# Performance work log

Measured on AMD Instinct MI355X. Metric: run time of the kernel, lower is better.

## Reference

```python
import jax, jax.numpy as jnp
import numpy as np
import math

NUM_BUCKETS = 32
MAX_DISTANCE = 128
N_HEADS = 16
HEAD_DIM = 64


def _relative_position_bucket(relative_position, num_buckets=NUM_BUCKETS, max_distance=MAX_DISTANCE):
    # bidirectional (encoder): half the buckets for positive positions
    nb = num_buckets // 2
    rel_buckets = (relative_position > 0).astype(jnp.int32) * nb
    rp = jnp.abs(relative_position)
    max_exact = nb // 2
    is_small = rp < max_exact
    rp_large = max_exact + (
        jnp.log(jnp.maximum(rp, 1).astype(jnp.float32) / max_exact)
        / math.log(max_distance / max_exact)
        * (nb - max_exact)
    ).astype(jnp.int32)
    rp_large = jnp.minimum(rp_large, nb - 1)
    return rel_buckets + jnp.where(is_small, rp, rp_large)


def setup_inputs() -> dict:
    key = jax.random.key(0)
    ks = jax.random.split(key, 6)
    d_model = 1024
    B, S = 4, 2048
    scale = 1.0 / math.sqrt(d_model)
    return {
        "hidden_states": jax.random.normal(ks[0], (B, S, d_model), jnp.float32),
        "Wq": jax.random.normal(ks[1], (d_model, N_HEADS * HEAD_DIM), jnp.float32) * scale,
        "Wk": jax.random.normal(ks[2], (d_model, N_HEADS * HEAD_DIM), jnp.float32) * scale,
        "Wv": jax.random.normal(ks[3], (d_model, N_HEADS * HEAD_DIM), jnp.float32) * scale,
        "Wo": jax.random.normal(ks[4], (N_HEADS * HEAD_DIM, d_model), jnp.float32) * scale,
        "rel_bias_table": jax.random.normal(ks[5], (NUM_BUCKETS, N_HEADS), jnp.float32),
    }


def reference(hidden_states, Wq, Wk, Wv, Wo, rel_bias_table):
    B, S, _ = hidden_states.shape
    # projections -> [B, H, S, hd]
    def proj(W):
        return jnp.einsum('bsd,df->bsf', hidden_states, W).reshape(B, S, N_HEADS, HEAD_DIM).transpose(0, 2, 1, 3)
    q = proj(Wq)
    k = proj(Wk)
    v = proj(Wv)

    # relative position bias: [1, H, S, S]
    ctx = jnp.arange(S)[:, None]
    mem = jnp.arange(S)[None, :]
    buckets = _relative_position_bucket(mem - ctx)  # [S, S] int32
    position_bias = rel_bias_table[buckets].transpose(2, 0, 1)[None]  # [1, H, S, S]

    # scaling = 1.0 in MT5Attention (d_kv**-0.5 baked into init elsewhere)
    attn_weights = jnp.einsum('bhqd,bhkd->bhqk', q, k) + position_bias
    attn_weights = jax.nn.softmax(attn_weights, axis=-1)
    attn_output = jnp.einsum('bhqk,bhkd->bqhd', attn_weights, v).reshape(B, S, N_HEADS * HEAD_DIM)
    attn_output = jnp.einsum('bsf,fd->bsd', attn_output, Wo)
    return attn_output, position_bias, attn_weights
```

## Files before the change

kernel.cpp:

```cpp
#include <hip/hip_runtime.h>
#include <cstdint>
#include <cmath>

#define NH 16
#define HD 64
#define SQ 2048
#define NB 4
#define DM 1024

typedef _Float16 half_t;
typedef _Float16 h8 __attribute__((ext_vector_type(8)));
typedef _Float16 h4 __attribute__((ext_vector_type(4)));
typedef float f4 __attribute__((ext_vector_type(4)));

__device__ __forceinline__ int rel_bucket(int delta) {
    int b = (delta > 0) ? 16 : 0;
    int a = (delta < 0) ? -delta : delta;
    if (a < 8) return b + a;
    int large = 8 + (int)(__logf((float)a * 0.125f) * 2.8853900817779268f);
    return b + (large < 15 ? large : 15);
}

__device__ __forceinline__ void gl_lds(const half_t* g, half_t* l) {
    __builtin_amdgcn_global_load_lds((const __attribute__((address_space(1))) unsigned int*)g,
                                     (__attribute__((address_space(3))) unsigned int*)l, 16, 0, 0);
}

__global__ __launch_bounds__(256) void prep(const float* __restrict__ X,
                                            const float* __restrict__ Wq,
                                            const float* __restrict__ Wk,
                                            const float* __restrict__ Wv,
                                            const float* __restrict__ Wo,
                                            const float* __restrict__ table,
                                            half_t* __restrict__ Xh, half_t* __restrict__ Wqt,
                                            half_t* __restrict__ Wkt, half_t* __restrict__ Wvt,
                                            half_t* __restrict__ Wot, float* __restrict__ dtab) {
    const int id = blockIdx.x;
    if (id < 4096) {
        size_t i = ((size_t)id * 256 + threadIdx.x) * 8;
        float4 a = *(const float4*)&X[i];
        float4 b = *(const float4*)&X[i + 4];
        half_t t[8] = {(half_t)a.x, (half_t)a.y, (half_t)a.z, (half_t)a.w,
                       (half_t)b.x, (half_t)b.y, (half_t)b.z, (half_t)b.w};
        *(h8*)&Xh[i] = *(h8*)t;
        return;
    }
    if (id >= 5120) {
        const int h = id - 5120;
        for (int d = threadIdx.x; d < 4095; d += 256)
            dtab[h * 4096 + d] = table[rel_bucket(d - 2047) * NH + h];
        return;
    }
    __shared__ float T[64][65];
    const int t = id - 4096;
    const int which = t >> 8, tile = t & 255;
    const float* W = which == 0 ? Wq : which == 1 ? Wk : which == 2 ? Wv : Wo;
    half_t* Wt = which == 0 ? Wqt : which == 1 ? Wkt : which == 2 ? Wvt : Wot;
    const int k0 = (tile >> 4) * 64, n0 = (tile & 15) * 64;
    const int c = threadIdx.x & 63, rr = threadIdx.x >> 6;
    for (int r = rr; r < 64; r += 4) T[r][c] = W[(size_t)(k0 + r) * DM + n0 + c];
    __syncthreads();
    for (int r = rr; r < 64; r += 4) Wt[(size_t)(n0 + r) * DM + k0 + c] = (half_t)T[c][r];
}

__global__ __launch_bounds__(256) void transpose_v(const half_t* __restrict__ v,
                                                   half_t* __restrict__ vT) {
    __shared__ half_t T[64][72];
    const int bh = blockIdx.y, j0 = blockIdx.x * 64;
    const size_t base = (size_t)bh * (SQ * HD);
    const int t = threadIdx.x;
    for (int e = t; e < 512; e += 256) {
        int r = e >> 3, c = e & 7;
        *(h8*)&T[r][c * 8] = *(const h8*)&v[base + (size_t)(j0 + r) * HD + c * 8];
    }
    __syncthreads();
    const int d = t & 63, jc = t >> 6;
    half_t tmp[16];
#pragma unroll
    for (int jj = 0; jj < 16; ++jj) tmp[jj] = T[jc * 16 + jj][d];
    *(h8*)&vT[base + (size_t)d * SQ + j0 + jc * 16] = *(h8*)&tmp[0];
    *(h8*)&vT[base + (size_t)d * SQ + j0 + jc * 16 + 8] = *(h8*)&tmp[8];
}

__global__ __launch_bounds__(256) void mm_qkv(const half_t* __restrict__ A,
                                              const half_t* __restrict__ Wqt,
                                              const half_t* __restrict__ Wkt,
                                              const half_t* __restrict__ Wvt,
                                              half_t* __restrict__ qo, half_t* __restrict__ ko,
                                              half_t* __restrict__ vo) {
    const int z = blockIdx.z;
    const half_t* Bt = z == 0 ? Wqt : z == 1 ? Wkt : Wvt;
    half_t* outp = z == 0 ? qo : z == 1 ? ko : vo;
    __shared__ half_t Al[2][4096];
    __shared__ half_t Bl[2][4096];
    const int tid = threadIdx.x;
    const int lane = tid & 63, w = tid >> 6;
    const int wr = w >> 1, wc = w & 1;
    const int id0 = blockIdx.y * 8 + blockIdx.x;
    const int swz = (id0 & 7) * 64 + (id0 >> 3);
    const int m0 = (swz >> 3) * 128, n0 = (swz & 7) * 128;

    f4 acc[4][4];
#pragma unroll
    for (int i = 0; i < 4; ++i)
#pragma unroll
        for (int j = 0; j < 4; ++j) acc[i][j] = (f4){0.f, 0.f, 0.f, 0.f};

    const int kc = lane >> 4;
    const int srl = lane >> 2;
    const int sc = lane & 3;

    auto stage = [&](int buf, int k0) {
#pragma unroll
        for (int inst = 0; inst < 2; ++inst) {
            int r = w * 32 + inst * 16 + srl;
            int cg = sc ^ ((r >> 1) & 3);
            gl_lds(&A[(size_t)(m0 + r) * DM + k0 + cg * 8], &Al[buf][(w * 32 + inst * 16) * 32]);
            gl_lds(&Bt[(size_t)(n0 + r) * DM + k0 + cg * 8], &Bl[buf][(w * 32 + inst * 16) * 32]);
        }
    };

    stage(0, 0);
    __syncthreads();
    int cur = 0;
    for (int t = 0; t < 32; ++t) {
        if (t < 31) stage(cur ^ 1, (t + 1) * 32);
        h8 af[4], bf[4];
#pragma unroll
        for (int ms = 0; ms < 4; ++ms) {
            int r = wr * 64 + ms * 16 + (lane & 15);
            af[ms] = *(const h8*)&Al[cur][r * 32 + ((kc ^ ((r >> 1) & 3)) * 8)];
        }
#pragma unroll
        for (int ns = 0; ns < 4; ++ns) {
            int r = wc * 64 + ns * 16 + (lane & 15);
            bf[ns] = *(const h8*)&Bl[cur][r * 32 + ((kc ^ ((r >> 1) & 3)) * 8)];
        }
#pragma unroll
        for (int ms = 0; ms < 4; ++ms)
#pragma unroll
            for (int ns = 0; ns < 4; ++ns)
                acc[ms][ns] =
                    __builtin_amdgcn_mfma_f32_16x16x32_f16(bf[ns], af[ms], acc[ms][ns], 0, 0, 0);
        __syncthreads();
        cur ^= 1;
    }

#pragma unroll
    for (int ms = 0; ms < 4; ++ms)
#pragma unroll
        for (int ns = 0; ns < 4; ++ns) {
            int m = m0 + wr * 64 + ms * 16 + (lane & 15);
            int nb = n0 + wc * 64 + ns * 16 + ((lane >> 4) << 2);
            int b = m >> 11, s = m & 2047, h = nb >> 6, d = nb & 63;
            h4 ph = {(half_t)acc[ms][ns][0], (half_t)acc[ms][ns][1], (half_t)acc[ms][ns][2],
                     (half_t)acc[ms][ns][3]};
            *(h4*)&outp[((size_t)(b * NH + h) * SQ + s) * HD + d] = ph;
        }
}

__global__ __launch_bounds__(256) void mm_wo(const half_t* __restrict__ A,
                                             const half_t* __restrict__ Bt,
                                             float* __restrict__ outp) {
    __shared__ half_t Al[2][4096];
    __shared__ half_t Bl[2][4096];
    const int tid = threadIdx.x;
    const int lane = tid & 63, w = tid >> 6;
    const int wr = w >> 1, wc = w & 1;
    const int id0 = blockIdx.y * 8 + blockIdx.x;
    const int swz = (id0 & 7) * 64 + (id0 >> 3);
    const int m0 = (swz >> 3) * 128, n0 = (swz & 7) * 128;

    f4 acc[4][4];
#pragma unroll
    for (int i = 0; i < 4; ++i)
#pragma unroll
        for (int j = 0; j < 4; ++j) acc[i][j] = (f4){0.f, 0.f, 0.f, 0.f};

    const int kc = lane >> 4;
    const int srl = lane >> 2;
    const int sc = lane & 3;

    auto stage = [&](int buf, int k0) {
#pragma unroll
        for (int inst = 0; inst < 2; ++inst) {
            int r = w * 32 + inst * 16 + srl;
            int cg = sc ^ ((r >> 1) & 3);
            gl_lds(&A[(size_t)(m0 + r) * DM + k0 + cg * 8], &Al[buf][(w * 32 + inst * 16) * 32]);
            gl_lds(&Bt[(size_t)(n0 + r) * DM + k0 + cg * 8], &Bl[buf][(w * 32 + inst * 16) * 32]);
        }
    };

    stage(0, 0);
    __syncthreads();
    int cur = 0;
    for (int t = 0; t < 32; ++t) {
        if (t < 31) stage(cur ^ 1, (t + 1) * 32);
        h8 af[4], bf[4];
#pragma unroll
        for (int ms = 0; ms < 4; ++ms) {
            int r = wr * 64 + ms * 16 + (lane & 15);
            af[ms] = *(const h8*)&Al[cur][r * 32 + ((kc ^ ((r >> 1) & 3)) * 8)];
        }
#pragma unroll
        for (int ns = 0; ns < 4; ++ns) {
            int r = wc * 64 + ns * 16 + (lane & 15);
            bf[ns] = *(const h8*)&Bl[cur][r * 32 + ((kc ^ ((r >> 1) & 3)) * 8)];
        }
#pragma unroll
        for (int ms = 0; ms < 4; ++ms)
#pragma unroll
            for (int ns = 0; ns < 4; ++ns)
                acc[ms][ns] =
                    __builtin_amdgcn_mfma_f32_16x16x32_f16(bf[ns], af[ms], acc[ms][ns], 0, 0, 0);
        __syncthreads();
        cur ^= 1;
    }

#pragma unroll
    for (int ms = 0; ms < 4; ++ms)
#pragma unroll
        for (int ns = 0; ns < 4; ++ns) {
            int m = m0 + wr * 64 + ms * 16 + (lane & 15);
            int nb = n0 + wc * 64 + ns * 16 + ((lane >> 4) << 2);
            __builtin_nontemporal_store(acc[ms][ns], (f4*)&outp[(size_t)m * DM + nb]);
        }
}

__global__ __launch_bounds__(256) void fused_attn(const half_t* __restrict__ q,
                                                  const half_t* __restrict__ k,
                                                  const half_t* __restrict__ vT,
                                                  const float* __restrict__ table,
                                                  float* __restrict__ attw,
                                                  half_t* __restrict__ ctx) {
    __shared__ float biasE[2176];
    __shared__ char Psm[16384];
    __shared__ half_t Kl[2][4096];
    __shared__ half_t Vl[2][4096];
    const int tid = threadIdx.x, lane = tid & 63, w = tid >> 6;

    const int id = blockIdx.x;
    const int idx = (id & 7) * 128 + (id >> 3);
    const int bh = idx >> 4, i0 = (idx & 15) * 128;
    const int h = bh & 15, b = bh >> 4;
    const size_t qb = (size_t)bh * (SQ * HD);
    const half_t* kb = k + qb;
    const half_t* vb = vT + qb;

    for (int t = tid; t < 2176; t += 256)
        biasE[t] = __expf(table[rel_bucket(t - i0 - 127) * NH + h]);

    h8 qf[2][2];
#pragma unroll
    for (int isub = 0; isub < 2; ++isub) {
        const half_t* qp =
            &q[qb + (size_t)(i0 + w * 32 + isub * 16 + (lane & 15)) * HD + (lane >> 4) * 8];
        qf[isub][0] = *(const h8*)qp;
        qf[isub][1] = *(const h8*)(qp + 32);
    }

    const int sr = lane >> 3;
    const int sc = lane & 7;

    auto stageK = [&](int buf, int j0) {
#pragma unroll
        for (int inst = 0; inst < 2; ++inst) {
            int r = w * 16 + inst * 8 + sr;
            gl_lds(&kb[(size_t)(j0 + r) * HD + ((sc ^ (r & 7)) * 8)],
                   &Kl[buf][(w * 16 + inst * 8) * 64]);
        }
    };
    auto stageV = [&](int buf, int j0) {
#pragma unroll
        for (int inst = 0; inst < 2; ++inst) {
            int r = w * 16 + inst * 8 + sr;
            gl_lds(&vb[(size_t)r * SQ + j0 + ((sc ^ (r & 7)) * 8)],
                   &Vl[buf][(w * 16 + inst * 8) * 64]);
        }
    };

    stageK(0, 0);
    __syncthreads();
    float srow[2] = {0.f, 0.f};
    int cur = 0;
    for (int t = 0; t < 32; ++t) {
        const int j0 = t * 64;
        if (t < 31) stageK(cur ^ 1, j0 + 64);
#pragma unroll
        for (int ns = 0; ns < 4; ++ns) {
            const int rr = ns * 16 + (lane & 15);
            const int kc = lane >> 4;
            h8 kf0 = *(const h8*)&Kl[cur][rr * 64 + ((kc ^ (rr & 7)) * 8)];
            h8 kf1 = *(const h8*)&Kl[cur][rr * 64 + (((kc + 4) ^ (rr & 7)) * 8)];
#pragma unroll
            for (int isub = 0; isub < 2; ++isub) {
                f4 z = (f4){0.f, 0.f, 0.f, 0.f};
                z = __builtin_amdgcn_mfma_f32_16x16x32_f16(kf0, qf[isub][0], z, 0, 0, 0);
                z = __builtin_amdgcn_mfma_f32_16x16x32_f16(kf1, qf[isub][1], z, 0, 0, 0);
                int u0 =
                    j0 + ns * 16 + ((lane >> 4) << 2) - (w * 32 + isub * 16 + (lane & 15)) + 127;
#pragma unroll
                for (int reg = 0; reg < 4; ++reg)
                    srow[isub] = fmaf(__expf(z[reg]), biasE[u0 + reg], srow[isub]);
            }
        }
        __syncthreads();
        cur ^= 1;
    }
    float sinv[2];
#pragma unroll
    for (int isub = 0; isub < 2; ++isub) {
        float s = srow[isub];
        s += __shfl_xor(s, 16);
        s += __shfl_xor(s, 32);
        sinv[isub] = 1.0f / s;
    }

    f4 o[4][2];
#pragma unroll
    for (int ns = 0; ns < 4; ++ns)
#pragma unroll
        for (int isub = 0; isub < 2; ++isub) o[ns][isub] = (f4){0.f, 0.f, 0.f, 0.f};
    const size_t awb = (size_t)bh * ((size_t)SQ * SQ);
    char* Pw = Psm + w * 4096;

    stageK(0, 0);
    stageV(0, 0);
    __syncthreads();
    cur = 0;
    for (int t = 0; t < 32; ++t) {
        const int j0 = t * 64;
        if (t < 31) {
            stageK(cur ^ 1, j0 + 64);
            stageV(cur ^ 1, j0 + 64);
        }
        __builtin_amdgcn_sched_barrier(0);
        f4 a[4][2];
#pragma unroll
        for (int ns = 0; ns < 4; ++ns) {
            const int rr = ns * 16 + (lane & 15);
            const int kc = lane >> 4;
            h8 kf0 = *(const h8*)&Kl[cur][rr * 64 + ((kc ^ (rr & 7)) * 8)];
            h8 kf1 = *(const h8*)&Kl[cur][rr * 64 + (((kc + 4) ^ (rr & 7)) * 8)];
#pragma unroll
            for (int isub = 0; isub < 2; ++isub) {
                f4 z = (f4){0.f, 0.f, 0.f, 0.f};
                z = __builtin_amdgcn_mfma_f32_16x16x32_f16(kf0, qf[isub][0], z, 0, 0, 0);
                z = __builtin_amdgcn_mfma_f32_16x16x32_f16(kf1, qf[isub][1], z, 0, 0, 0);
                a[ns][isub] = z;
            }
        }
#pragma unroll
        for (int ns = 0; ns < 4; ++ns)
#pragma unroll
            for (int isub = 0; isub < 2; ++isub) {
                const int wloc = w * 32 + isub * 16 + (lane & 15);
                const int jbase = ns * 16 + ((lane >> 4) << 2);
                const int u0 = j0 + jbase - wloc + 127;
                f4 p;
#pragma unroll
                for (int reg = 0; reg < 4; ++reg)
                    p[reg] = __expf(a[ns][isub][reg]) * biasE[u0 + reg] * sinv[isub];
                __builtin_nontemporal_store(p,
                                            (f4*)&attw[awb + (size_t)(i0 + wloc) * SQ + j0 + jbase]);
                const int iloc = isub * 16 + (lane & 15);
                h4 ph = {(half_t)p[0], (half_t)p[1], (half_t)p[2], (half_t)p[3]};
                *(h4*)&Pw[iloc * 128 + (((jbase >> 3) ^ (iloc & 7)) << 4) + ((jbase & 4) << 1)] = ph;
            }
        h8 pf[2][2];
#pragma unroll
        for (int isub = 0; isub < 2; ++isub) {
            const int iloc = isub * 16 + (lane & 15);
            pf[isub][0] = *(const h8*)&Pw[iloc * 128 + (((lane >> 4) ^ (iloc & 7)) << 4)];
            pf[isub][1] = *(const h8*)&Pw[iloc * 128 + ((((lane >> 4) + 4) ^ (iloc & 7)) << 4)];
        }
#pragma unroll
        for (int ns = 0; ns < 4; ++ns) {
            const int rr = ns * 16 + (lane & 15);
            const int kc = lane >> 4;
            h8 vf0 = *(const h8*)&Vl[cur][rr * 64 + ((kc ^ (rr & 7)) * 8)];
            h8 vf1 = *(const h8*)&Vl[cur][rr * 64 + (((kc + 4) ^ (rr & 7)) * 8)];
#pragma unroll
            for (int isub = 0; isub < 2; ++isub) {
                o[ns][isub] =
                    __builtin_amdgcn_mfma_f32_16x16x32_f16(pf[isub][0], vf0, o[ns][isub], 0, 0, 0);
                o[ns][isub] =
                    __builtin_amdgcn_mfma_f32_16x16x32_f16(pf[isub][1], vf1, o[ns][isub], 0, 0, 0);
            }
        }
        asm volatile("s_waitcnt vmcnt(8)" ::: "memory");
        __builtin_amdgcn_s_barrier();
        __builtin_amdgcn_sched_barrier(0);
        cur ^= 1;
    }
#pragma unroll
    for (int ns = 0; ns < 4; ++ns)
#pragma unroll
        for (int isub = 0; isub < 2; ++isub)
#pragma unroll
            for (int reg = 0; reg < 4; ++reg) {
                int row = i0 + w * 32 + isub * 16 + (lane >> 4) * 4 + reg;
                int d = ns * 16 + (lane & 15);
                ctx[((size_t)(b * SQ + row)) * DM + h * HD + d] = (half_t)o[ns][isub][reg];
            }
}

__global__ __launch_bounds__(256) void bias_fill(const float* __restrict__ dtab,
                                                 float* __restrict__ pb) {
    __shared__ float L[2052];
    const int i = blockIdx.x, h = blockIdx.y;
    const int s0 = 2047 - i, a0 = s0 & ~3, sh = s0 - a0;
    for (int t = threadIdx.x * 4; t < 2052; t += 1024)
        *(f4*)&L[t] = *(const f4*)&dtab[h * 4096 + a0 + t];
    __syncthreads();
    const size_t base = ((size_t)h * SQ + i) * SQ;
#pragma unroll
    for (int half = 0; half < 2; ++half) {
        int j = half * 1024 + threadIdx.x * 4;
        f4 o = {L[sh + j], L[sh + j + 1], L[sh + j + 2], L[sh + j + 3]};
        __builtin_nontemporal_store(o, (f4*)&pb[base + j]);
    }
}

extern "C" void kernel_launch(void* const* d_in, const int* in_sizes, int n_in, void* d_out,
                              int out_size, void* d_ws, size_t ws_size, hipStream_t stream) {
    const float* X = (const float*)d_in[0];
    const float* Wq = (const float*)d_in[1];
    const float* Wk = (const float*)d_in[2];
    const float* Wv = (const float*)d_in[3];
    const float* Wo = (const float*)d_in[4];
    const float* tbl = (const float*)d_in[5];

    float* out = (float*)d_out;
    float* attn_out = out;
    float* pb = out + (size_t)NB * SQ * DM;
    float* attw = pb + (size_t)NH * SQ * SQ;

    const size_t need_bytes = 109314048;
    half_t* hb = (ws_size >= need_bytes) ? (half_t*)d_ws : (half_t*)pb;
    half_t* Xh = hb;
    half_t* qh = hb + 8388608;
    half_t* kh = hb + 16777216;
    half_t* vh = hb + 25165824;
    half_t* vTh = hb + 33554432;
    half_t* ctxh = hb + 41943040;
    half_t* Wqt = hb + 50331648;
    half_t* Wkt = hb + 51380224;
    half_t* Wvt = hb + 52428800;
    half_t* Wot = hb + 53477376;
    float* dtab = (float*)(hb + 54525952);

    dim3 blk(256);
    prep<<<dim3(5136), blk, 0, stream>>>(X, Wq, Wk, Wv, Wo, tbl, Xh, Wqt, Wkt, Wvt, Wot, dtab);
    mm_qkv<<<dim3(8, 64, 3), blk, 0, stream>>>(Xh, Wqt, Wkt, Wvt, qh, kh, vh);
    transpose_v<<<dim3(32, 64), blk, 0, stream>>>(vh, vTh);
    fused_attn<<<dim3(1024), blk, 0, stream>>>(qh, kh, vTh, tbl, attw, ctxh);
    mm_wo<<<dim3(8, 64), blk, 0, stream>>>(ctxh, Wot, attn_out);
    bias_fill<<<dim3(SQ, NH), blk, 0, stream>>>(dtab, pb);
}
```

Measured before the change: 542.6 us.

## Fuse V transpose into QKV GEMM, keep P in registers, merge Wo with bias fill

The QKV GEMM now writes V directly in transposed layout for the z==2 slice, so the separate transpose kernel is gone. The attention kernel keeps P in registers by permuting the K row layout to match the MFMA operand pattern, which removes the LDS P round trip and frees 16KB of shared memory. It also reads precomputed exp-bias entries from dtab and sets launch bounds for 3 blocks per CU. The Wo GEMM and the position-bias fill are merged into one launch so the memory-bound fill can overlap the GEMM; the swizzle changes raise the risk of layout bugs.

```diff
diff --git a/kernel.cpp b/kernel.cpp
--- a/kernel.cpp
+++ b/kernel.cpp
@@ -11,6 +11,7 @@
 typedef _Float16 half_t;
 typedef _Float16 h8 __attribute__((ext_vector_type(8)));
 typedef _Float16 h4 __attribute__((ext_vector_type(4)));
+typedef _Float16 h2 __attribute__((ext_vector_type(2)));
 typedef float f4 __attribute__((ext_vector_type(4)));
 
 __device__ __forceinline__ int rel_bucket(int delta) {
@@ -25,6 +26,16 @@
     __builtin_amdgcn_global_load_lds((const __attribute__((address_space(1))) unsigned int*)g,
                                      (__attribute__((address_space(3))) unsigned int*)l, 16, 0, 0);
 }
+
+__device__ __forceinline__ h2 pkrtz(float a, float b) {
+    auto r = __builtin_amdgcn_cvt_pkrtz(a, b);
+    return *(h2*)&r;
+}
+
+union PFU {
+    h2 x[4];
+    h8 v;
+};
 
 __global__ __launch_bounds__(256) void prep(const float* __restrict__ X,
                                             const float* __restrict__ Wq,
@@ -47,7 +58,7 @@
     }
     if (id >= 5120) {
         const int h = id - 5120;
-        for (int d = threadIdx.x; d < 4095; d += 256)
+        for (int d = threadIdx.x; d < 4096; d += 256)
             dtab[h * 4096 + d] = table[rel_bucket(d - 2047) * NH + h];
         return;
     }
@@ -63,34 +74,14 @@
     for (int r = rr; r < 64; r += 4) Wt[(size_t)(n0 + r) * DM + k0 + c] = (half_t)T[c][r];
 }
 
-__global__ __launch_bounds__(256) void transpose_v(const half_t* __restrict__ v,
-                                                   half_t* __restrict__ vT) {
-    __shared__ half_t T[64][72];
-    const int bh = blockIdx.y, j0 = blockIdx.x * 64;
-    const size_t base = (size_t)bh * (SQ * HD);
-    const int t = threadIdx.x;
-    for (int e = t; e < 512; e += 256) {
-        int r = e >> 3, c = e & 7;
-        *(h8*)&T[r][c * 8] = *(const h8*)&v[base + (size_t)(j0 + r) * HD + c * 8];
-    }
-    __syncthreads();
-    const int d = t & 63, jc = t >> 6;
-    half_t tmp[16];
-#pragma unroll
-    for (int jj = 0; jj < 16; ++jj) tmp[jj] = T[jc * 16 + jj][d];
-    *(h8*)&vT[base + (size_t)d * SQ + j0 + jc * 16] = *(h8*)&tmp[0];
-    *(h8*)&vT[base + (size_t)d * SQ + j0 + jc * 16 + 8] = *(h8*)&tmp[8];
-}
-
 __global__ __launch_bounds__(256) void mm_qkv(const half_t* __restrict__ A,
                                               const half_t* __restrict__ Wqt,
                                               const half_t* __restrict__ Wkt,
                                               const half_t* __restrict__ Wvt,
                                               half_t* __restrict__ qo, half_t* __restrict__ ko,
-                                              half_t* __restrict__ vo) {
+                                              half_t* __restrict__ vTo) {
     const int z = blockIdx.z;
-    const half_t* Bt = z == 0 ? Wqt : z == 1 ? Wkt : Wvt;
-    half_t* outp = z == 0 ? qo : z == 1 ? ko : vo;
+    const half_t* Bt = z == 0 ? Wqt : (z == 1 ? Wkt : Wvt);
     __shared__ half_t Al[2][4096];
     __shared__ half_t Bl[2][4096];
     const int tid = threadIdx.x;
@@ -100,12 +91,6 @@
     const int swz = (id0 & 7) * 64 + (id0 >> 3);
     const int m0 = (swz >> 3) * 128, n0 = (swz & 7) * 128;
 
-    f4 acc[4][4];
-#pragma unroll
-    for (int i = 0; i < 4; ++i)
-#pragma unroll
-        for (int j = 0; j < 4; ++j) acc[i][j] = (f4){0.f, 0.f, 0.f, 0.f};
-
     const int kc = lane >> 4;
     const int srl = lane >> 2;
     const int sc = lane & 3;
@@ -120,121 +105,94 @@
         }
     };
 
+    f4 acc[4][4];
+#pragma unroll
+    for (int i = 0; i < 4; ++i)
+#pragma unroll
+        for (int j = 0; j < 4; ++j) acc[i][j] = (f4){0.f, 0.f, 0.f, 0.f};
+
     stage(0, 0);
     __syncthreads();
     int cur = 0;
-    for (int t = 0; t < 32; ++t) {
-        if (t < 31) stage(cur ^ 1, (t + 1) * 32);
-        h8 af[4], bf[4];
-#pragma unroll
-        for (int ms = 0; ms < 4; ++ms) {
-            int r = wr * 64 + ms * 16 + (lane & 15);
-            af[ms] = *(const h8*)&Al[cur][r * 32 + ((kc ^ ((r >> 1) & 3)) * 8)];
-        }
-#pragma unroll
-        for (int ns = 0; ns < 4; ++ns) {
-            int r = wc * 64 + ns * 16 + (lane & 15);
-            bf[ns] = *(const h8*)&Bl[cur][r * 32 + ((kc ^ ((r >> 1) & 3)) * 8)];
-        }
+    if (z < 2) {
+        for (int t = 0; t < 32; ++t) {
+            if (t < 31) stage(cur ^ 1, (t + 1) * 32);
+            h8 af[4], bf[4];
+#pragma unroll
+            for (int ms = 0; ms < 4; ++ms) {
+                int r = wr * 64 + ms * 16 + (lane & 15);
+                af[ms] = *(const h8*)&Al[cur][r * 32 + ((kc ^ ((r >> 1) & 3)) * 8)];
+            }
+#pragma unroll
+            for (int ns = 0; ns < 4; ++ns) {
+                int r = wc * 64 + ns * 16 + (lane & 15);
+                bf[ns] = *(const h8*)&Bl[cur][r * 32 + ((kc ^ ((r >> 1) & 3)) * 8)];
+            }
+#pragma unroll
+            for (int ms = 0; ms < 4; ++ms)
+#pragma unroll
+                for (int ns = 0; ns < 4; ++ns)
+                    acc[ms][ns] = __builtin_amdgcn_mfma_f32_16x16x32_f16(bf[ns], af[ms],
+                                                                         acc[ms][ns], 0, 0, 0);
+            __syncthreads();
+            cur ^= 1;
+        }
+        half_t* outp = z == 0 ? qo : ko;
 #pragma unroll
         for (int ms = 0; ms < 4; ++ms)
 #pragma unroll
-            for (int ns = 0; ns < 4; ++ns)
-                acc[ms][ns] =
-                    __builtin_amdgcn_mfma_f32_16x16x32_f16(bf[ns], af[ms], acc[ms][ns], 0, 0, 0);
-        __syncthreads();
-        cur ^= 1;
-    }
-
-#pragma unroll
-    for (int ms = 0; ms < 4; ++ms)
-#pragma unroll
-        for (int ns = 0; ns < 4; ++ns) {
-            int m = m0 + wr * 64 + ms * 16 + (lane & 15);
-            int nb = n0 + wc * 64 + ns * 16 + ((lane >> 4) << 2);
-            int b = m >> 11, s = m & 2047, h = nb >> 6, d = nb & 63;
-            h4 ph = {(half_t)acc[ms][ns][0], (half_t)acc[ms][ns][1], (half_t)acc[ms][ns][2],
-                     (half_t)acc[ms][ns][3]};
-            *(h4*)&outp[((size_t)(b * NH + h) * SQ + s) * HD + d] = ph;
-        }
-}
-
-__global__ __launch_bounds__(256) void mm_wo(const half_t* __restrict__ A,
-                                             const half_t* __restrict__ Bt,
-                                             float* __restrict__ outp) {
-    __shared__ half_t Al[2][4096];
-    __shared__ half_t Bl[2][4096];
-    const int tid = threadIdx.x;
-    const int lane = tid & 63, w = tid >> 6;
-    const int wr = w >> 1, wc = w & 1;
-    const int id0 = blockIdx.y * 8 + blockIdx.x;
-    const int swz = (id0 & 7) * 64 + (id0 >> 3);
-    const int m0 = (swz >> 3) * 128, n0 = (swz & 7) * 128;
-
-    f4 acc[4][4];
-#pragma unroll
-    for (int i = 0; i < 4; ++i)
-#pragma unroll
-        for (int j = 0; j < 4; ++j) acc[i][j] = (f4){0.f, 0.f, 0.f, 0.f};
-
-    const int kc = lane >> 4;
-    const int srl = lane >> 2;
-    const int sc = lane & 3;
-
-    auto stage = [&](int buf, int k0) {
-#pragma unroll
-        for (int inst = 0; inst < 2; ++inst) {
-            int r = w * 32 + inst * 16 + srl;
-            int cg = sc ^ ((r >> 1) & 3);
-            gl_lds(&A[(size_t)(m0 + r) * DM + k0 + cg * 8], &Al[buf][(w * 32 + inst * 16) * 32]);
-            gl_lds(&Bt[(size_t)(n0 + r) * DM + k0 + cg * 8], &Bl[buf][(w * 32 + inst * 16) * 32]);
-        }
-    };
-
-    stage(0, 0);
-    __syncthreads();
-    int cur = 0;
-    for (int t = 0; t < 32; ++t) {
-        if (t < 31) stage(cur ^ 1, (t + 1) * 32);
-        h8 af[4], bf[4];
-#pragma unroll
-        for (int ms = 0; ms < 4; ++ms) {
-            int r = wr * 64 + ms * 16 + (lane & 15);
-            af[ms] = *(const h8*)&Al[cur][r * 32 + ((kc ^ ((r >> 1) & 3)) * 8)];
-        }
-#pragma unroll
-        for (int ns = 0; ns < 4; ++ns) {
-            int r = wc * 64 + ns * 16 + (lane & 15);
-            bf[ns] = *(const h8*)&Bl[cur][r * 32 + ((kc ^ ((r >> 1) & 3)) * 8)];
+            for (int ns = 0; ns < 4; ++ns) {
+                int m = m0 + wr * 64 + ms * 16 + (lane & 15);
+                int nb = n0 + wc * 64 + ns * 16 + ((lane >> 4) << 2);
+                int b = m >> 11, s = m & 2047, h = nb >> 6, d = nb & 63;
+                h4 ph = {(half_t)acc[ms][ns][0], (half_t)acc[ms][ns][1], (half_t)acc[ms][ns][2],
+                         (half_t)acc[ms][ns][3]};
+                *(h4*)&outp[((size_t)(b * NH + h) * SQ + s) * HD + d] = ph;
+            }
+    } else {
+        for (int t = 0; t < 32; ++t) {
+            if (t < 31) stage(cur ^ 1, (t + 1) * 32);
+            h8 af[4], bf[4];
+#pragma unroll
+            for (int ms = 0; ms < 4; ++ms) {
+                int r = wr * 64 + ms * 16 + (lane & 15);
+                af[ms] = *(const h8*)&Al[cur][r * 32 + ((kc ^ ((r >> 1) & 3)) * 8)];
+            }
+#pragma unroll
+            for (int ns = 0; ns < 4; ++ns) {
+                int r = wc * 64 + ns * 16 + (lane & 15);
+                bf[ns] = *(const h8*)&Bl[cur][r * 32 + ((kc ^ ((r >> 1) & 3)) * 8)];
+            }
+#pragma unroll
+            for (int ms = 0; ms < 4; ++ms)
+#pragma unroll
+                for (int ns = 0; ns < 4; ++ns)
+                    acc[ms][ns] = __builtin_amdgcn_mfma_f32_16x16x32_f16(af[ms], bf[ns],
+                                                                         acc[ms][ns], 0, 0, 0);
+            __syncthreads();
+            cur ^= 1;
         }
 #pragma unroll
         for (int ms = 0; ms < 4; ++ms)
 #pragma unroll
-            for (int ns = 0; ns < 4; ++ns)
-                acc[ms][ns] =
-                    __builtin_amdgcn_mfma_f32_16x16x32_f16(bf[ns], af[ms], acc[ms][ns], 0, 0, 0);
-        __syncthreads();
-        cur ^= 1;
-    }
-
-#pragma unroll
-    for (int ms = 0; ms < 4; ++ms)
-#pragma unroll
-        for (int ns = 0; ns < 4; ++ns) {
-            int m = m0 + wr * 64 + ms * 16 + (lane & 15);
-            int nb = n0 + wc * 64 + ns * 16 + ((lane >> 4) << 2);
-            __builtin_nontemporal_store(acc[ms][ns], (f4*)&outp[(size_t)m * DM + nb]);
-        }
-}
-
-__global__ __launch_bounds__(256) void fused_attn(const half_t* __restrict__ q,
-                                                  const half_t* __restrict__ k,
-                                                  const half_t* __restrict__ vT,
-                                                  const float* __restrict__ table,
-                                                  float* __restrict__ attw,
-                                                  half_t* __restrict__ ctx) {
+            for (int ns = 0; ns < 4; ++ns) {
+                int s = m0 + wr * 64 + ms * 16 + ((lane >> 4) << 2);
+                int nb = n0 + wc * 64 + ns * 16 + (lane & 15);
+                int b = s >> 11, sl = s & 2047, h = nb >> 6, d = nb & 63;
+                h4 ph = {(half_t)acc[ms][ns][0], (half_t)acc[ms][ns][1], (half_t)acc[ms][ns][2],
+                         (half_t)acc[ms][ns][3]};
+                *(h4*)&vTo[((size_t)(b * NH + h) * HD + d) * SQ + sl] = ph;
+            }
+    }
+}
+
+__global__ __launch_bounds__(256, 3) void fused_attn(const half_t* __restrict__ q,
+                                                     const half_t* __restrict__ k,
+                                                     const half_t* __restrict__ vT,
+                                                     const float* __restrict__ dtab,
+                                                     float* __restrict__ attw,
+                                                     half_t* __restrict__ ctx) {
     __shared__ float biasE[2176];
-    __shared__ char Psm[16384];
     __shared__ half_t Kl[2][4096];
     __shared__ half_t Vl[2][4096];
     const int tid = threadIdx.x, lane = tid & 63, w = tid >> 6;
@@ -247,8 +205,7 @@
     const half_t* kb = k + qb;
     const half_t* vb = vT + qb;
 
-    for (int t = tid; t < 2176; t += 256)
-        biasE[t] = __expf(table[rel_bucket(t - i0 - 127) * NH + h]);
+    for (int t = tid; t < 2176; t += 256) biasE[t] = __expf(dtab[h * 4096 + t - i0 + 1920]);
 
     h8 qf[2][2];
 #pragma unroll
@@ -261,23 +218,26 @@
 
     const int sr = lane >> 3;
     const int sc = lane & 7;
+    const int kc = lane >> 4;
+    const int f_s0 = 0 + ((lane >> 3) & 3);
+    const int f_s1 = 4 + ((lane >> 3) & 3);
+    const int f_k = (((lane >> 2) & 1) << 2) + (lane & 3);
+    const int f_v = (((lane >> 3) & 1) << 2) + (lane & 3);
+    const int rb64 = ((((lane & 15) >> 2) << 3) + (lane & 3)) << 6;
 
     auto stageK = [&](int buf, int j0) {
-#pragma unroll
-        for (int inst = 0; inst < 2; ++inst) {
-            int r = w * 16 + inst * 8 + sr;
-            gl_lds(&kb[(size_t)(j0 + r) * HD + ((sc ^ (r & 7)) * 8)],
-                   &Kl[buf][(w * 16 + inst * 8) * 64]);
-        }
+        int r0 = w * 16 + sr;
+        gl_lds(&kb[(size_t)(j0 + r0) * HD + ((sc ^ f_s0) * 8)], &Kl[buf][(w * 16) * 64]);
+        gl_lds(&kb[(size_t)(j0 + r0 + 8) * HD + ((sc ^ f_s1) * 8)], &Kl[buf][(w * 16 + 8) * 64]);
     };
     auto stageV = [&](int buf, int j0) {
-#pragma unroll
-        for (int inst = 0; inst < 2; ++inst) {
-            int r = w * 16 + inst * 8 + sr;
-            gl_lds(&vb[(size_t)r * SQ + j0 + ((sc ^ (r & 7)) * 8)],
-                   &Vl[buf][(w * 16 + inst * 8) * 64]);
-        }
+        int r0 = w * 16 + sr;
+        gl_lds(&vb[(size_t)r0 * SQ + j0 + ((sc ^ f_s0) * 8)], &Vl[buf][(w * 16) * 64]);
+        gl_lds(&vb[(size_t)(r0 + 8) * SQ + j0 + ((sc ^ f_s1) * 8)], &Vl[buf][(w * 16 + 8) * 64]);
     };
+
+    const int il0 = w * 32 + (lane & 15);
+    const int c8 = (lane >> 4) << 3;
 
     stageK(0, 0);
     __syncthreads();
@@ -288,17 +248,16 @@
         if (t < 31) stageK(cur ^ 1, j0 + 64);
 #pragma unroll
         for (int ns = 0; ns < 4; ++ns) {
-            const int rr = ns * 16 + (lane & 15);
-            const int kc = lane >> 4;
-            h8 kf0 = *(const h8*)&Kl[cur][rr * 64 + ((kc ^ (rr & 7)) * 8)];
-            h8 kf1 = *(const h8*)&Kl[cur][rr * 64 + (((kc + 4) ^ (rr & 7)) * 8)];
+            const int roff = rb64 + (((ns >> 1) * 32 + (ns & 1) * 4) << 6);
+            h8 kf0 = *(const h8*)&Kl[cur][roff + ((kc ^ f_k) * 8)];
+            h8 kf1 = *(const h8*)&Kl[cur][roff + (((kc + 4) ^ f_k) * 8)];
 #pragma unroll
             for (int isub = 0; isub < 2; ++isub) {
                 f4 z = (f4){0.f, 0.f, 0.f, 0.f};
                 z = __builtin_amdgcn_mfma_f32_16x16x32_f16(kf0, qf[isub][0], z, 0, 0, 0);
                 z = __builtin_amdgcn_mfma_f32_16x16x32_f16(kf1, qf[isub][1], z, 0, 0, 0);
-                int u0 =
-                    j0 + ns * 16 + ((lane >> 4) << 2) - (w * 32 + isub * 16 + (lane & 15)) + 127;
+                const int u0 =
+                    j0 + (ns >> 1) * 32 + c8 + (ns & 1) * 4 - (il0 + isub * 16) + 127;
 #pragma unroll
                 for (int reg = 0; reg < 4; ++reg)
                     srow[isub] = fmaf(__expf(z[reg]), biasE[u0 + reg], srow[isub]);
@@ -322,7 +281,6 @@
 #pragma unroll
         for (int isub = 0; isub < 2; ++isub) o[ns][isub] = (f4){0.f, 0.f, 0.f, 0.f};
     const size_t awb = (size_t)bh * ((size_t)SQ * SQ);
-    char* Pw = Psm + w * 4096;
 
     stageK(0, 0);
     stageV(0, 0);
@@ -335,57 +293,40 @@
             stageV(cur ^ 1, j0 + 64);
         }
         __builtin_amdgcn_sched_barrier(0);
-        f4 a[4][2];
+        PFU pf[2][2];
 #pragma unroll
         for (int ns = 0; ns < 4; ++ns) {
-            const int rr = ns * 16 + (lane & 15);
-            const int kc = lane >> 4;
-            h8 kf0 = *(const h8*)&Kl[cur][rr * 64 + ((kc ^ (rr & 7)) * 8)];
-            h8 kf1 = *(const h8*)&Kl[cur][rr * 64 + (((kc + 4) ^ (rr & 7)) * 8)];
+            const int roff = rb64 + (((ns >> 1) * 32 + (ns & 1) * 4) << 6);
+            h8 kf0 = *(const h8*)&Kl[cur][roff + ((kc ^ f_k) * 8)];
+            h8 kf1 = *(const h8*)&Kl[cur][roff + (((kc + 4) ^ f_k) * 8)];
 #pragma unroll
             for (int isub = 0; isub < 2; ++isub) {
                 f4 z = (f4){0.f, 0.f, 0.f, 0.f};
                 z = __builtin_amdgcn_mfma_f32_16x16x32_f16(kf0, qf[isub][0], z, 0, 0, 0);
                 z = __builtin_amdgcn_mfma_f32_16x16x32_f16(kf1, qf[isub][1], z, 0, 0, 0);
-                a[ns][isub] = z;
-            }
-        }
-#pragma unroll
-        for (int ns = 0; ns < 4; ++ns)
-#pragma unroll
-            for (int isub = 0; isub < 2; ++isub) {
-                const int wloc = w * 32 + isub * 16 + (lane & 15);
-                const int jbase = ns * 16 + ((lane >> 4) << 2);
-                const int u0 = j0 + jbase - wloc + 127;
+                const int jl = (ns >> 1) * 32 + c8 + (ns & 1) * 4;
+                const int u0 = j0 + jl - (il0 + isub * 16) + 127;
                 f4 p;
 #pragma unroll
                 for (int reg = 0; reg < 4; ++reg)
-                    p[reg] = __expf(a[ns][isub][reg]) * biasE[u0 + reg] * sinv[isub];
-                __builtin_nontemporal_store(p,
-                                            (f4*)&attw[awb + (size_t)(i0 + wloc) * SQ + j0 + jbase]);
-                const int iloc = isub * 16 + (lane & 15);
-                h4 ph = {(half_t)p[0], (half_t)p[1], (half_t)p[2], (half_t)p[3]};
-                *(h4*)&Pw[iloc * 128 + (((jbase >> 3) ^ (iloc & 7)) << 4) + ((jbase & 4) << 1)] = ph;
-            }
-        h8 pf[2][2];
-#pragma unroll
-        for (int isub = 0; isub < 2; ++isub) {
-            const int iloc = isub * 16 + (lane & 15);
-            pf[isub][0] = *(const h8*)&Pw[iloc * 128 + (((lane >> 4) ^ (iloc & 7)) << 4)];
-            pf[isub][1] = *(const h8*)&Pw[iloc * 128 + ((((lane >> 4) + 4) ^ (iloc & 7)) << 4)];
+                    p[reg] = __expf(z[reg]) * biasE[u0 + reg] * sinv[isub];
+                __builtin_nontemporal_store(
+                    p, (f4*)&attw[awb + (size_t)(i0 + il0 + isub * 16) * SQ + j0 + jl]);
+                pf[isub][ns >> 1].x[(ns & 1) * 2 + 0] = pkrtz(p[0], p[1]);
+                pf[isub][ns >> 1].x[(ns & 1) * 2 + 1] = pkrtz(p[2], p[3]);
+            }
         }
 #pragma unroll
         for (int ns = 0; ns < 4; ++ns) {
             const int rr = ns * 16 + (lane & 15);
-            const int kc = lane >> 4;
-            h8 vf0 = *(const h8*)&Vl[cur][rr * 64 + ((kc ^ (rr & 7)) * 8)];
-            h8 vf1 = *(const h8*)&Vl[cur][rr * 64 + (((kc + 4) ^ (rr & 7)) * 8)];
+            h8 vf0 = *(const h8*)&Vl[cur][rr * 64 + ((kc ^ f_v) * 8)];
+            h8 vf1 = *(const h8*)&Vl[cur][rr * 64 + (((kc + 4) ^ f_v) * 8)];
 #pragma unroll
             for (int isub = 0; isub < 2; ++isub) {
-                o[ns][isub] =
-                    __builtin_amdgcn_mfma_f32_16x16x32_f16(pf[isub][0], vf0, o[ns][isub], 0, 0, 0);
-                o[ns][isub] =
-                    __builtin_amdgcn_mfma_f32_16x16x32_f16(pf[isub][1], vf1, o[ns][isub], 0, 0, 0);
+                o[ns][isub] = __builtin_amdgcn_mfma_f32_16x16x32_f16(pf[isub][0].v, vf0,
+                                                                    o[ns][isub], 0, 0, 0);
+                o[ns][isub] = __builtin_amdgcn_mfma_f32_16x16x32_f16(pf[isub][1].v, vf1,
+                                                                    o[ns][isub], 0, 0, 0);
             }
         }
         asm volatile("s_waitcnt vmcnt(8)" ::: "memory");
@@ -403,6 +344,94 @@
                 int d = ns * 16 + (lane & 15);
                 ctx[((size_t)(b * SQ + row)) * DM + h * HD + d] = (half_t)o[ns][isub][reg];
             }
+}
+
+__global__ __launch_bounds__(256) void wo_bias(const half_t* __restrict__ A,
+                                               const half_t* __restrict__ Bt,
+                                               float* __restrict__ outp,
+                                               const float* __restrict__ dtab,
+                                               float* __restrict__ pb) {
+    __shared__ char SM[32768];
+    if (blockIdx.x >= 512) {
+        float* L = (float*)SM;
+        const int id = blockIdx.x - 512;
+        const int h = id >> 11, i = id & 2047;
+        const int s0 = 2047 - i, a0 = s0 & ~3, sh = s0 - a0;
+        for (int t = threadIdx.x * 4; t < 2052; t += 1024)
+            *(f4*)&L[t] = *(const f4*)&dtab[h * 4096 + a0 + t];
+        __syncthreads();
+        const size_t base = ((size_t)h * SQ + i) * SQ;
+#pragma unroll
+        for (int half = 0; half < 2; ++half) {
+            int j = half * 1024 + threadIdx.x * 4;
+            f4 o = {L[sh + j], L[sh + j + 1], L[sh + j + 2], L[sh + j + 3]};
+            __builtin_nontemporal_store(o, (f4*)&pb[base + j]);
+        }
+        return;
+    }
+    half_t(*Al)[4096] = (half_t(*)[4096])SM;
+    half_t(*Bl)[4096] = (half_t(*)[4096])(SM + 16384);
+    const int tid = threadIdx.x;
+    const int lane = tid & 63, w = tid >> 6;
+    const int wr = w >> 1, wc = w & 1;
+    const int id0 = blockIdx.x;
+    const int swz = (id0 & 7) * 64 + (id0 >> 3);
+    const int m0 = (swz >> 3) * 128, n0 = (swz & 7) * 128;
+
+    f4 acc[4][4];
+#pragma unroll
+    for (int i = 0; i < 4; ++i)
+#pragma unroll
+        for (int j = 0; j < 4; ++j) acc[i][j] = (f4){0.f, 0.f, 0.f, 0.f};
+
+    const int kc = lane >> 4;
+    const int srl = lane >> 2;
+    const int sc = lane & 3;
+
+    auto stage = [&](int buf, int k0) {
+#pragma unroll
+        for (int inst = 0; inst < 2; ++inst) {
+            int r = w * 32 + inst * 16 + srl;
+            int cg = sc ^ ((r >> 1) & 3);
+            gl_lds(&A[(size_t)(m0 + r) * DM + k0 + cg * 8], &Al[buf][(w * 32 + inst * 16) * 32]);
+            gl_lds(&Bt[(size_t)(n0 + r) * DM + k0 + cg * 8], &Bl[buf][(w * 32 + inst * 16) * 32]);
+        }
+    };
+
+    stage(0, 0);
+    __syncthreads();
+    int cur = 0;
+    for (int t = 0; t < 32; ++t) {
+        if (t < 31) stage(cur ^ 1, (t + 1) * 32);
+        h8 af[4], bf[4];
+#pragma unroll
+        for (int ms = 0; ms < 4; ++ms) {
+            int r = wr * 64 + ms * 16 + (lane & 15);
+            af[ms] = *(const h8*)&Al[cur][r * 32 + ((kc ^ ((r >> 1) & 3)) * 8)];
+        }
+#pragma unroll
+        for (int ns = 0; ns < 4; ++ns) {
+            int r = wc * 64 + ns * 16 + (lane & 15);
+            bf[ns] = *(const h8*)&Bl[cur][r * 32 + ((kc ^ ((r >> 1) & 3)) * 8)];
+        }
+#pragma unroll
+        for (int ms = 0; ms < 4; ++ms)
+#pragma unroll
+            for (int ns = 0; ns < 4; ++ns)
+                acc[ms][ns] =
+                    __builtin_amdgcn_mfma_f32_16x16x32_f16(bf[ns], af[ms], acc[ms][ns], 0, 0, 0);
+        __syncthreads();
+        cur ^= 1;
+    }
+
+#pragma unroll
+    for (int ms = 0; ms < 4; ++ms)
+#pragma unroll
+        for (int ns = 0; ns < 4; ++ns) {
+            int m = m0 + wr * 64 + ms * 16 + (lane & 15);
+            int nb = n0 + wc * 64 + ns * 16 + ((lane >> 4) << 2);
+            __builtin_nontemporal_store(acc[ms][ns], (f4*)&outp[(size_t)m * DM + nb]);
+        }
 }
 
 __global__ __launch_bounds__(256) void bias_fill(const float* __restrict__ dtab,
@@ -437,11 +466,11 @@
     float* attw = pb + (size_t)NH * SQ * SQ;
 
     const size_t need_bytes = 109314048;
-    half_t* hb = (ws_size >= need_bytes) ? (half_t*)d_ws : (half_t*)pb;
+    const bool ws_ok = (ws_size >= need_bytes);
+    half_t* hb = ws_ok ? (half_t*)d_ws : (half_t*)pb;
     half_t* Xh = hb;
     half_t* qh = hb + 8388608;
     half_t* kh = hb + 16777216;
-    half_t* vh = hb + 25165824;
     half_t* vTh = hb + 33554432;
     half_t* ctxh = hb + 41943040;
     half_t* Wqt = hb + 50331648;
@@ -452,9 +481,12 @@
 
     dim3 blk(256);
     prep<<<dim3(5136), blk, 0, stream>>>(X, Wq, Wk, Wv, Wo, tbl, Xh, Wqt, Wkt, Wvt, Wot, dtab);
-    mm_qkv<<<dim3(8, 64, 3), blk, 0, stream>>>(Xh, Wqt, Wkt, Wvt, qh, kh, vh);
-    transpose_v<<<dim3(32, 64), blk, 0, stream>>>(vh, vTh);
-    fused_attn<<<dim3(1024), blk, 0, stream>>>(qh, kh, vTh, tbl, attw, ctxh);
-    mm_wo<<<dim3(8, 64), blk, 0, stream>>>(ctxh, Wot, attn_out);
-    bias_fill<<<dim3(SQ, NH), blk, 0, stream>>>(dtab, pb);
-}
+    mm_qkv<<<dim3(8, 64, 3), blk, 0, stream>>>(Xh, Wqt, Wkt, Wvt, qh, kh, vTh);
+    fused_attn<<<dim3(1024), blk, 0, stream>>>(qh, kh, vTh, dtab, attw, ctxh);
+    if (ws_ok) {
+        wo_bias<<<dim3(512 + 32768), blk, 0, stream>>>(ctxh, Wot, attn_out, dtab, pb);
+    } else {
+        wo_bias<<<dim3(512), blk, 0, stream>>>(ctxh, Wot, attn_out, dtab, pb);
+        bias_fill<<<dim3(SQ, NH), blk, 0, stream>>>(dtab, pb);
+    }
+}
```

After: 909.7 us. +67.6%, slower.
